# Kernel tuning notes

Measured on AMD Instinct MI355X. Metric: run time of the kernel, lower is better.

Reference implementation:

```python
import jax, jax.numpy as jnp
import numpy as np

B, S, D, DS = 8, 2048, 1024, 128
TEMP = 1.0
C = 8.0


def setup_inputs() -> dict:
    key = jax.random.key(0)
    ks = jax.random.split(key, 8)
    s_in = 1.0 / np.sqrt(D)
    s_st = 1.0 / np.sqrt(DS)
    return {
        "x": jax.random.normal(ks[0], (B, S, D), jnp.float32),
        "W_k": jax.random.normal(ks[1], (DS, D), jnp.float32) * s_in,
        "W_v": jax.random.normal(ks[2], (DS, D), jnp.float32) * s_in,
        "W_q": jax.random.normal(ks[3], (DS, D), jnp.float32) * s_in,
        "W_alpha_w": jax.random.normal(ks[4], (DS, D), jnp.float32) * s_in,
        "W_alpha_b": jnp.zeros((DS,), jnp.float32),
        "lambda_param": jax.random.uniform(ks[5], (DS,), jnp.float32, 4.0, 9.0),
        "W_o": jax.random.normal(ks[6], (D, DS), jnp.float32) * s_st,
        "norm_weight": jnp.ones((DS,), jnp.float32),
    }


def _l2norm(z):
    # matches F.normalize(..., dim=-1) with eps=1e-12
    n = jnp.linalg.norm(z, axis=-1, keepdims=True)
    return z / jnp.maximum(n, 1e-12)


def reference(x, W_k, W_v, W_q, W_alpha_w, W_alpha_b, lambda_param, W_o, norm_weight):
    # projections
    k = _l2norm(x @ W_k.T)                      # [B,S,DS]
    v = x @ W_v.T                               # [B,S,DS]
    q = _l2norm(x @ W_q.T)                      # [B,S,DS]
    r = jax.nn.sigmoid(x @ W_alpha_w.T + W_alpha_b)
    log_a = jnp.log(jax.nn.sigmoid(lambda_param) + 1e-8)  # [DS]
    alpha = jnp.exp(C * r * log_a)              # [B,S,DS], data-dependent decay

    H0 = jnp.zeros((B, DS, DS), x.dtype)        # state indexed [b, k, v]

    def step(H, inp):
        k_t, v_t, q_t, a_t = inp                # each [B,DS]
        # surprise: prediction error against current state
        pred = jnp.einsum('bk,bkv->bv', q_t, H)
        err = jnp.sum((v_t - pred) ** 2, axis=-1, keepdims=True)  # [B,1]
        sur = jax.nn.sigmoid(err / (TEMP + 1e-6))                 # [B,1]
        # delta rule: k (x) v - k (x) (k^T H) = k (x) (v - k^T H)
        k_proj = jnp.einsum('bk,bkv->bv', k_t, H)
        delta = k_t[:, :, None] * (v_t - k_proj)[:, None, :]      # [B,DS,DS]
        a_e = a_t[:, :, None]                                     # decay on k-axis
        H = a_e * H + (1.0 - a_e) * (sur[:, :, None] * delta)
        y = jnp.einsum('bk,bkv->bv', q_t, H)
        return H, y

    seq = (k.transpose(1, 0, 2), v.transpose(1, 0, 2),
           q.transpose(1, 0, 2), alpha.transpose(1, 0, 2))
    _, ys = jax.lax.scan(step, H0, seq)         # ys: [S,B,DS]
    y = ys.transpose(1, 0, 2)                   # [B,S,DS]

    # RMSNorm (computed in fp32, like the torch module)
    yf = y.astype(jnp.float32)
    yn = yf * jax.lax.rsqrt(jnp.mean(yf * yf, axis=-1, keepdims=True) + 1e-6)
    yn = (yn * norm_weight).astype(y.dtype)
    return yn @ W_o.T                           # [B,S,D]
```

## Files before the change

### kernel.cpp

```cpp
#include <hip/hip_runtime.h>
#include <math.h>

#define S_LEN 2048
#define B_SZ 8
#define D_IN 1024
#define DS_ 128
#define INV_TEMP (1.0f/1.000001f)

__global__ __launch_bounds__(256) void proj_gemm(
    const float* __restrict__ X,
    const float* __restrict__ Wk, const float* __restrict__ Wv,
    const float* __restrict__ Wq, const float* __restrict__ Wa,
    float* __restrict__ P)
{
    __shared__ __align__(16) float As[32][68];
    __shared__ __align__(16) float Bs[32][68];
    const int tid = threadIdx.x;
    const int m0 = blockIdx.x * 64;
    const int n0 = blockIdx.y * 64;
    const int lr = tid >> 3;
    const int lk4 = tid & 7;

    const float* wrows[2];
#pragma unroll
    for (int i = 0; i < 2; i++) {
        int nn = n0 + lr + i * 32;
        const float* w;
        if      (nn < 128) w = Wk + (size_t)nn * D_IN;
        else if (nn < 256) w = Wv + (size_t)(nn - 128) * D_IN;
        else if (nn < 384) w = Wq + (size_t)(nn - 256) * D_IN;
        else               w = Wa + (size_t)(nn - 384) * D_IN;
        wrows[i] = w;
    }
    const int ty = tid >> 4, tx = tid & 15;
    float acc[4][4];
#pragma unroll
    for (int i = 0; i < 4; i++)
#pragma unroll
        for (int j = 0; j < 4; j++) acc[i][j] = 0.f;

    for (int k0 = 0; k0 < D_IN; k0 += 32) {
#pragma unroll
        for (int i = 0; i < 2; i++) {
            int m = lr + i * 32;
            float4 a4 = *(const float4*)(X + (size_t)(m0 + m) * D_IN + k0 + lk4 * 4);
            As[lk4*4+0][m] = a4.x; As[lk4*4+1][m] = a4.y;
            As[lk4*4+2][m] = a4.z; As[lk4*4+3][m] = a4.w;
            float4 b4 = *(const float4*)(wrows[i] + k0 + lk4 * 4);
            Bs[lk4*4+0][m] = b4.x; Bs[lk4*4+1][m] = b4.y;
            Bs[lk4*4+2][m] = b4.z; Bs[lk4*4+3][m] = b4.w;
        }
        __syncthreads();
#pragma unroll
        for (int kk = 0; kk < 32; kk++) {
            float4 a4 = *(const float4*)(&As[kk][ty * 4]);
            float4 b4 = *(const float4*)(&Bs[kk][tx * 4]);
            float a[4] = {a4.x, a4.y, a4.z, a4.w};
            float b[4] = {b4.x, b4.y, b4.z, b4.w};
#pragma unroll
            for (int i = 0; i < 4; i++)
#pragma unroll
                for (int j = 0; j < 4; j++)
                    acc[i][j] = fmaf(a[i], b[j], acc[i][j]);
        }
        __syncthreads();
    }
#pragma unroll
    for (int i = 0; i < 4; i++) {
        float4 o; o.x = acc[i][0]; o.y = acc[i][1]; o.z = acc[i][2]; o.w = acc[i][3];
        *(float4*)(P + (size_t)(m0 + ty * 4 + i) * 512 + n0 + tx * 4) = o;
    }
}

__global__ __launch_bounds__(128) void postproc(
    float* __restrict__ P, float* __restrict__ G,
    const float* __restrict__ bA, const float* __restrict__ lam)
{
    const int tok = blockIdx.x, i = threadIdx.x;
    float* row = P + (size_t)tok * 512;
    float kr = row[i], qr = row[256 + i], rr = row[384 + i];
    float ks = kr * kr, qs = qr * qr;
#pragma unroll
    for (int m = 1; m < 64; m <<= 1) { ks += __shfl_xor(ks, m); qs += __shfl_xor(qs, m); }
    __shared__ float sb[6];
    if ((i & 63) == 0) { sb[(i >> 6) * 2] = ks; sb[(i >> 6) * 2 + 1] = qs; }
    __syncthreads();
    float kinv = 1.0f / fmaxf(sqrtf(sb[0] + sb[2]), 1e-12f);
    float qinv = 1.0f / fmaxf(sqrtf(sb[1] + sb[3]), 1e-12f);
    float kn = kr * kinv, qn = qr * qinv;
    float sr = 1.0f / (1.0f + __expf(-(rr + bA[i])));
    float sl = 1.0f / (1.0f + __expf(-lam[i]));
    float la = logf(sl + 1e-8f);
    float al = __expf(8.0f * sr * la);
    row[i]       = kn;
    row[256 + i] = qn;
    row[384 + i] = al;
    float gi = qn * (1.0f - al) * kn;
#pragma unroll
    for (int m = 1; m < 64; m <<= 1) gi += __shfl_xor(gi, m);
    if ((i & 63) == 0) sb[4 + (i >> 6)] = gi;
    __syncthreads();
    if (i == 0) G[tok] = sb[4] + sb[5];
}

__global__ __launch_bounds__(512, 2) void recurrence(
    const float* __restrict__ P, const float* __restrict__ G, float* __restrict__ Y)
{
    const int b = blockIdx.x;
    const int tid = threadIdx.x;
    const int c = tid & 7;
    const int vp = tid >> 3;
    const int lane = tid & 63;
    const int wave = tid >> 6;

    __shared__ __align__(16) float Pbuf[3][808];
    __shared__ __align__(16) float errw[2][8];

    const float* Pb = P + (size_t)b * S_LEN * 512;
    const float* Gb = G + (size_t)b * S_LEN;
    float* Yb = Y + (size_t)b * S_LEN * DS_;

    float H0[16], H1[16];
#pragma unroll
    for (int j = 0; j < 16; j++) { H0[j] = 0.f; H1[j] = 0.f; }

    const bool isP = tid < 256;
    const bool isG = (tid == 256);
    int spos = 0;
    if (isP) {
        int i0 = tid * 2, sec = i0 >> 7, idx = i0 & 127;
        spos = sec * 160 + (idx >> 4) * 20 + (idx & 15);
    }
    const int voff = 160 + (vp >> 3) * 20 + ((2 * vp) & 15);

    float2 rp0, rp1; float rg0 = 0.f, rg1 = 0.f;
    if (isP) {
        rp0 = *(const float2*)(Pb + tid * 2);
        rp1 = *(const float2*)(Pb + 512 + tid * 2);
    }
    if (isG) { rg0 = Gb[0]; rg1 = Gb[1]; }
    if (isP) *(float2*)(&Pbuf[0][spos]) = rp0;
    if (isG) Pbuf[0][800] = rg0;
    __syncthreads();

#define DOTC(j, u, comp) { \
    float q_ = q4[j].comp, k_ = k4[j].comp, a_ = a4[j].comp; \
    float h0 = H0[(j)*4+(u)], h1 = H1[(j)*4+(u)]; \
    pr0 = fmaf(q_, h0, pr0); pr1 = fmaf(q_, h1, pr1); \
    kp0 = fmaf(k_, h0, kp0); kp1 = fmaf(k_, h1, kp1); \
    float qa_ = q_ * a_; \
    ya0 = fmaf(qa_, h0, ya0); ya1 = fmaf(qa_, h1, ya1); }

#define UPDC(j, u, comp) { \
    float k_ = k4[j].comp, a_ = a4[j].comp; \
    float t0 = k_ * sd0, t1 = k_ * sd1; \
    H0[(j)*4+(u)] = fmaf(a_, H0[(j)*4+(u)] - t0, t0); \
    H1[(j)*4+(u)] = fmaf(a_, H1[(j)*4+(u)] - t1, t1); }

#define STEP(T, PAR, RPS, RGS, RPL, RGL) { \
    float* cb = &Pbuf[(T) % 3][0]; \
    const float* bk = cb + c * 20; \
    float4 k4[4], q4[4], a4[4]; \
    _Pragma("unroll") for (int j = 0; j < 4; j++) { \
        k4[j] = *(const float4*)(bk + j * 4); \
        q4[j] = *(const float4*)(bk + 320 + j * 4); \
        a4[j] = *(const float4*)(bk + 480 + j * 4); } \
    float2 vt = *(const float2*)(cb + voff); \
    float g = cb[800]; \
    float pr0 = 0, pr1 = 0, kp0 = 0, kp1 = 0, ya0 = 0, ya1 = 0; \
    _Pragma("unroll") for (int j = 0; j < 4; j++) { \
        DOTC(j, 0, x) DOTC(j, 1, y) DOTC(j, 2, z) DOTC(j, 3, w) } \
    _Pragma("unroll") for (int m = 1; m <= 4; m <<= 1) { \
        pr0 += __shfl_xor(pr0, m); pr1 += __shfl_xor(pr1, m); \
        kp0 += __shfl_xor(kp0, m); kp1 += __shfl_xor(kp1, m); \
        ya0 += __shfl_xor(ya0, m); ya1 += __shfl_xor(ya1, m); } \
    float e0 = vt.x - pr0, e1 = vt.y - pr1; \
    float d0 = vt.x - kp0, d1 = vt.y - kp1; \
    float ep = fmaf(e0, e0, e1 * e1); \
    ep += __shfl_xor(ep, 8); ep += __shfl_xor(ep, 16); ep += __shfl_xor(ep, 32); \
    if (lane == 0) errw[PAR][wave] = ep; \
    if ((T) + 1 < S_LEN) { \
        if (isP) *(float2*)(&Pbuf[((T) + 1) % 3][spos]) = RPS; \
        if (isG) Pbuf[((T) + 1) % 3][800] = RGS; } \
    if ((T) + 2 < S_LEN) { \
        if (isP) RPL = *(const float2*)(Pb + (size_t)((T) + 2) * 512 + tid * 2); \
        if (isG) RGL = Gb[(T) + 2]; } \
    __syncthreads(); \
    float4 ea = *(const float4*)(&errw[PAR][0]); \
    float4 eb = *(const float4*)(&errw[PAR][4]); \
    float err = ((ea.x + ea.y) + (ea.z + ea.w)) + ((eb.x + eb.y) + (eb.z + eb.w)); \
    float sur = 1.0f / (1.0f + __expf(-err * INV_TEMP)); \
    float sd0 = sur * d0, sd1 = sur * d1; \
    if (c == 0) { \
        float2 yv; float sg = sur * g; \
        yv.x = fmaf(sg, d0, ya0); yv.y = fmaf(sg, d1, ya1); \
        *(float2*)(Yb + (size_t)(T) * DS_ + vp * 2) = yv; } \
    _Pragma("unroll") for (int j = 0; j < 4; j++) { \
        UPDC(j, 0, x) UPDC(j, 1, y) UPDC(j, 2, z) UPDC(j, 3, w) } \
}

    for (int t = 0; t < S_LEN; t += 2) {
        STEP(t,     0, rp1, rg1, rp0, rg0)
        STEP(t + 1, 1, rp0, rg0, rp1, rg1)
    }
#undef DOTC
#undef UPDC
#undef STEP
}

__global__ __launch_bounds__(128) void rmsnorm(
    const float* __restrict__ Y, const float* __restrict__ nw, float* __restrict__ Yn)
{
    const int tok = blockIdx.x, i = threadIdx.x;
    float y = Y[(size_t)tok * DS_ + i];
    float s = y * y;
#pragma unroll
    for (int m = 1; m < 64; m <<= 1) s += __shfl_xor(s, m);
    __shared__ float sb[2];
    if ((i & 63) == 0) sb[i >> 6] = s;
    __syncthreads();
    float ms = (sb[0] + sb[1]) * (1.0f / 128.0f);
    Yn[(size_t)tok * DS_ + i] = y * rsqrtf(ms + 1e-6f) * nw[i];
}

__global__ __launch_bounds__(256) void out_gemm(
    const float* __restrict__ Yn, const float* __restrict__ Wo, float* __restrict__ Out)
{
    __shared__ __align__(16) float As[32][68];
    __shared__ __align__(16) float Bs[32][68];
    const int tid = threadIdx.x;
    const int m0 = blockIdx.x * 64;
    const int n0 = blockIdx.y * 64;
    const int lr = tid >> 3;
    const int lk4 = tid & 7;
    const int ty = tid >> 4, tx = tid & 15;
    float acc[4][4];
#pragma unroll
    for (int i = 0; i < 4; i++)
#pragma unroll
        for (int j = 0; j < 4; j++) acc[i][j] = 0.f;

    for (int k0 = 0; k0 < DS_; k0 += 32) {
#pragma unroll
        for (int i = 0; i < 2; i++) {
            int m = lr + i * 32;
            float4 a4 = *(const float4*)(Yn + (size_t)(m0 + m) * DS_ + k0 + lk4 * 4);
            As[lk4*4+0][m] = a4.x; As[lk4*4+1][m] = a4.y;
            As[lk4*4+2][m] = a4.z; As[lk4*4+3][m] = a4.w;
            float4 b4 = *(const float4*)(Wo + (size_t)(n0 + m) * DS_ + k0 + lk4 * 4);
            Bs[lk4*4+0][m] = b4.x; Bs[lk4*4+1][m] = b4.y;
            Bs[lk4*4+2][m] = b4.z; Bs[lk4*4+3][m] = b4.w;
        }
        __syncthreads();
#pragma unroll
        for (int kk = 0; kk < 32; kk++) {
            float4 a4 = *(const float4*)(&As[kk][ty * 4]);
            float4 b4 = *(const float4*)(&Bs[kk][tx * 4]);
            float a[4] = {a4.x, a4.y, a4.z, a4.w};
            float b[4] = {b4.x, b4.y, b4.z, b4.w};
#pragma unroll
            for (int i = 0; i < 4; i++)
#pragma unroll
                for (int j = 0; j < 4; j++)
                    acc[i][j] = fmaf(a[i], b[j], acc[i][j]);
        }
        __syncthreads();
    }
#pragma unroll
    for (int i = 0; i < 4; i++) {
        float4 o; o.x = acc[i][0]; o.y = acc[i][1]; o.z = acc[i][2]; o.w = acc[i][3];
        *(float4*)(Out + (size_t)(m0 + ty * 4 + i) * 1024 + n0 + tx * 4) = o;
    }
}

extern "C" void kernel_launch(void* const* d_in, const int* in_sizes, int n_in,
                              void* d_out, int out_size, void* d_ws, size_t ws_size,
                              hipStream_t stream)
{
    const float* x   = (const float*)d_in[0];
    const float* Wk  = (const float*)d_in[1];
    const float* Wv  = (const float*)d_in[2];
    const float* Wq  = (const float*)d_in[3];
    const float* Waw = (const float*)d_in[4];
    const float* Wab = (const float*)d_in[5];
    const float* lam = (const float*)d_in[6];
    const float* Wo  = (const float*)d_in[7];
    const float* nw  = (const float*)d_in[8];
    float* out = (float*)d_out;

    const size_t NTOK = (size_t)B_SZ * S_LEN;
    float* P  = (float*)d_ws;
    float* Y  = P + NTOK * 512;
    float* Yn = Y + NTOK * DS_;
    float* G  = Yn + NTOK * DS_;

    proj_gemm<<<dim3(NTOK / 64, 512 / 64), 256, 0, stream>>>(x, Wk, Wv, Wq, Waw, P);
    postproc<<<NTOK, 128, 0, stream>>>(P, G, Wab, lam);
    recurrence<<<B_SZ, 512, 0, stream>>>(P, G, Y);
    rmsnorm<<<NTOK, 128, 0, stream>>>(Y, nw, Yn);
    out_gemm<<<dim3(NTOK / 64, 1024 / 64), 256, 0, stream>>>(Yn, Wo, out);
}
```

Before: 3.003 ms.

## Precompute q*alpha and k*(1-alpha) and remap recurrence thread layout to 16x4

postproc now also writes per-token q*alpha, k*(1-alpha) and the gate scalar into a second buffer, so the recurrence no longer forms these products each step. The recurrence changes its thread mapping from 8 k-chunks by 2 v columns to 16 k-chunks by 4 v columns, with the H slice held as float4 registers, a padded shared-memory layout, and the decay/weight loads moved after the error reduction. rmsnorm writes in place to drop a buffer. The cost is more global traffic per step and longer shuffle reductions (16 lanes instead of 8).

```diff
diff --git a/kernel.cpp b/kernel.cpp
--- a/kernel.cpp
+++ b/kernel.cpp
@@ -6,6 +6,8 @@
 #define D_IN 1024
 #define DS_ 128
 #define INV_TEMP (1.0f/1.000001f)
+#define QROW 260
+#define LBUF 1092
 
 __global__ __launch_bounds__(256) void proj_gemm(
     const float* __restrict__ X,
@@ -73,7 +75,7 @@
 }
 
 __global__ __launch_bounds__(128) void postproc(
-    float* __restrict__ P, float* __restrict__ G,
+    float* __restrict__ P, float* __restrict__ Q2,
     const float* __restrict__ bA, const float* __restrict__ lam)
 {
     const int tok = blockIdx.x, i = threadIdx.x;
@@ -92,124 +94,130 @@
     float sl = 1.0f / (1.0f + __expf(-lam[i]));
     float la = logf(sl + 1e-8f);
     float al = __expf(8.0f * sr * la);
-    row[i]       = kn;
-    row[256 + i] = qn;
-    row[384 + i] = al;
+    row[i] = kn; row[256 + i] = qn; row[384 + i] = al;
+    float* q2 = Q2 + (size_t)tok * QROW;
+    q2[i] = qn * al;
+    q2[128 + i] = kn * (1.0f - al);
     float gi = qn * (1.0f - al) * kn;
 #pragma unroll
     for (int m = 1; m < 64; m <<= 1) gi += __shfl_xor(gi, m);
     if ((i & 63) == 0) sb[4 + (i >> 6)] = gi;
     __syncthreads();
-    if (i == 0) G[tok] = sb[4] + sb[5];
+    if (i == 0) q2[256] = sb[4] + sb[5];
 }
 
 __global__ __launch_bounds__(512, 2) void recurrence(
-    const float* __restrict__ P, const float* __restrict__ G, float* __restrict__ Y)
+    const float* __restrict__ P, const float* __restrict__ Q2, float* __restrict__ Y)
 {
     const int b = blockIdx.x;
     const int tid = threadIdx.x;
-    const int c = tid & 7;
-    const int vp = tid >> 3;
+    const int c = tid & 15;
+    const int vp = tid >> 4;
     const int lane = tid & 63;
     const int wave = tid >> 6;
-
-    __shared__ __align__(16) float Pbuf[3][808];
+    const int co = c * 12;
+
+    __shared__ __align__(16) float Pbuf[3][LBUF];
     __shared__ __align__(16) float errw[2][8];
 
     const float* Pb = P + (size_t)b * S_LEN * 512;
-    const float* Gb = G + (size_t)b * S_LEN;
+    const float* Qb = Q2 + (size_t)b * S_LEN * QROW;
     float* Yb = Y + (size_t)b * S_LEN * DS_;
 
-    float H0[16], H1[16];
-#pragma unroll
-    for (int j = 0; j < 16; j++) { H0[j] = 0.f; H1[j] = 0.f; }
-
-    const bool isP = tid < 256;
-    const bool isG = (tid == 256);
-    int spos = 0;
-    if (isP) {
-        int i0 = tid * 2, sec = i0 >> 7, idx = i0 & 127;
-        spos = sec * 160 + (idx >> 4) * 20 + (idx & 15);
-    }
-    const int voff = 160 + (vp >> 3) * 20 + ((2 * vp) & 15);
-
-    float2 rp0, rp1; float rg0 = 0.f, rg1 = 0.f;
-    if (isP) {
-        rp0 = *(const float2*)(Pb + tid * 2);
-        rp1 = *(const float2*)(Pb + 512 + tid * 2);
-    }
-    if (isG) { rg0 = Gb[0]; rg1 = Gb[1]; }
-    if (isP) *(float2*)(&Pbuf[0][spos]) = rp0;
-    if (isG) Pbuf[0][800] = rg0;
+    float4 H0={0,0,0,0},H1={0,0,0,0},H2={0,0,0,0},H3={0,0,0,0},
+           H4={0,0,0,0},H5={0,0,0,0},H6={0,0,0,0},H7={0,0,0,0};
+
+    const bool isS = tid < 385;
+    int spos = 0; const float* src = nullptr; int sstr = 0;
+    if (tid < 256) {
+        int i = tid * 2, s = i >> 7, idx = i & 127, cp = (idx >> 3) * 12 + (idx & 7);
+        spos = (s == 0) ? cp : (s == 1) ? (960 + idx) : (s == 2) ? (192 + cp) : (576 + cp);
+        src = Pb + i; sstr = 512;
+    } else if (tid < 385) {
+        int i2 = (tid - 256) * 2, s = i2 >> 7, idx = i2 & 127, cp = (idx >> 3) * 12 + (idx & 7);
+        spos = (tid == 384) ? 1088 : ((s == 0) ? (384 + cp) : (768 + cp));
+        src = Qb + i2; sstr = QROW;
+    }
+
+    float2 r0 = {0.f, 0.f}, r1 = {0.f, 0.f};
+    if (isS) { r0 = *(const float2*)(src); r1 = *(const float2*)(src + sstr); }
+    if (isS) *(float2*)(&Pbuf[0][spos]) = r0;
     __syncthreads();
 
-#define DOTC(j, u, comp) { \
-    float q_ = q4[j].comp, k_ = k4[j].comp, a_ = a4[j].comp; \
-    float h0 = H0[(j)*4+(u)], h1 = H1[(j)*4+(u)]; \
-    pr0 = fmaf(q_, h0, pr0); pr1 = fmaf(q_, h1, pr1); \
-    kp0 = fmaf(k_, h0, kp0); kp1 = fmaf(k_, h1, kp1); \
-    float qa_ = q_ * a_; \
-    ya0 = fmaf(qa_, h0, ya0); ya1 = fmaf(qa_, h1, ya1); }
-
-#define UPDC(j, u, comp) { \
-    float k_ = k4[j].comp, a_ = a4[j].comp; \
-    float t0 = k_ * sd0, t1 = k_ * sd1; \
-    H0[(j)*4+(u)] = fmaf(a_, H0[(j)*4+(u)] - t0, t0); \
-    H1[(j)*4+(u)] = fmaf(a_, H1[(j)*4+(u)] - t1, t1); }
-
-#define STEP(T, PAR, RPS, RGS, RPL, RGL) { \
+#define RED16(v4) { _Pragma("unroll") for (int m_ = 1; m_ < 16; m_ <<= 1) { \
+    v4.x += __shfl_xor(v4.x, m_); v4.y += __shfl_xor(v4.y, m_); \
+    v4.z += __shfl_xor(v4.z, m_); v4.w += __shfl_xor(v4.w, m_); } }
+
+#define DOTJ(qs, ks, zs, Hj) { \
+    pr.x = fmaf(qs, Hj.x, pr.x); pr.y = fmaf(qs, Hj.y, pr.y); \
+    pr.z = fmaf(qs, Hj.z, pr.z); pr.w = fmaf(qs, Hj.w, pr.w); \
+    kp.x = fmaf(ks, Hj.x, kp.x); kp.y = fmaf(ks, Hj.y, kp.y); \
+    kp.z = fmaf(ks, Hj.z, kp.z); kp.w = fmaf(ks, Hj.w, kp.w); \
+    ya.x = fmaf(zs, Hj.x, ya.x); ya.y = fmaf(zs, Hj.y, ya.y); \
+    ya.z = fmaf(zs, Hj.z, ya.z); ya.w = fmaf(zs, Hj.w, ya.w); }
+
+#define UPDJ(as_, ws_, Hj) { \
+    Hj.x = fmaf(as_, Hj.x, ws_ * sd.x); Hj.y = fmaf(as_, Hj.y, ws_ * sd.y); \
+    Hj.z = fmaf(as_, Hj.z, ws_ * sd.z); Hj.w = fmaf(as_, Hj.w, ws_ * sd.w); }
+
+#define STEP(T, PAR, RS_, RL_) { \
     float* cb = &Pbuf[(T) % 3][0]; \
-    const float* bk = cb + c * 20; \
-    float4 k4[4], q4[4], a4[4]; \
-    _Pragma("unroll") for (int j = 0; j < 4; j++) { \
-        k4[j] = *(const float4*)(bk + j * 4); \
-        q4[j] = *(const float4*)(bk + 320 + j * 4); \
-        a4[j] = *(const float4*)(bk + 480 + j * 4); } \
-    float2 vt = *(const float2*)(cb + voff); \
-    float g = cb[800]; \
-    float pr0 = 0, pr1 = 0, kp0 = 0, kp1 = 0, ya0 = 0, ya1 = 0; \
-    _Pragma("unroll") for (int j = 0; j < 4; j++) { \
-        DOTC(j, 0, x) DOTC(j, 1, y) DOTC(j, 2, z) DOTC(j, 3, w) } \
-    _Pragma("unroll") for (int m = 1; m <= 4; m <<= 1) { \
-        pr0 += __shfl_xor(pr0, m); pr1 += __shfl_xor(pr1, m); \
-        kp0 += __shfl_xor(kp0, m); kp1 += __shfl_xor(kp1, m); \
-        ya0 += __shfl_xor(ya0, m); ya1 += __shfl_xor(ya1, m); } \
-    float e0 = vt.x - pr0, e1 = vt.y - pr1; \
-    float d0 = vt.x - kp0, d1 = vt.y - kp1; \
-    float ep = fmaf(e0, e0, e1 * e1); \
-    ep += __shfl_xor(ep, 8); ep += __shfl_xor(ep, 16); ep += __shfl_xor(ep, 32); \
+    const float4 k0 = *(const float4*)(cb + co); \
+    const float4 k1 = *(const float4*)(cb + co + 4); \
+    const float4 q0 = *(const float4*)(cb + 192 + co); \
+    const float4 q1 = *(const float4*)(cb + 192 + co + 4); \
+    const float4 z0 = *(const float4*)(cb + 384 + co); \
+    const float4 z1 = *(const float4*)(cb + 384 + co + 4); \
+    const float4 vt = *(const float4*)(cb + 960 + vp * 4); \
+    const float g = cb[1088]; \
+    float4 pr = {0,0,0,0}, kp = {0,0,0,0}, ya = {0,0,0,0}; \
+    DOTJ(q0.x, k0.x, z0.x, H0) DOTJ(q0.y, k0.y, z0.y, H1) \
+    DOTJ(q0.z, k0.z, z0.z, H2) DOTJ(q0.w, k0.w, z0.w, H3) \
+    DOTJ(q1.x, k1.x, z1.x, H4) DOTJ(q1.y, k1.y, z1.y, H5) \
+    DOTJ(q1.z, k1.z, z1.z, H6) DOTJ(q1.w, k1.w, z1.w, H7) \
+    RED16(pr) RED16(kp) RED16(ya) \
+    float4 d4; d4.x = vt.x - kp.x; d4.y = vt.y - kp.y; \
+    d4.z = vt.z - kp.z; d4.w = vt.w - kp.w; \
+    float ex = vt.x - pr.x, ey = vt.y - pr.y, ez = vt.z - pr.z, ew = vt.w - pr.w; \
+    float ep = fmaf(ex, ex, fmaf(ey, ey, fmaf(ez, ez, ew * ew))); \
+    ep += __shfl_xor(ep, 16); ep += __shfl_xor(ep, 32); \
     if (lane == 0) errw[PAR][wave] = ep; \
-    if ((T) + 1 < S_LEN) { \
-        if (isP) *(float2*)(&Pbuf[((T) + 1) % 3][spos]) = RPS; \
-        if (isG) Pbuf[((T) + 1) % 3][800] = RGS; } \
-    if ((T) + 2 < S_LEN) { \
-        if (isP) RPL = *(const float2*)(Pb + (size_t)((T) + 2) * 512 + tid * 2); \
-        if (isG) RGL = Gb[(T) + 2]; } \
+    if ((T) + 1 < S_LEN && isS) *(float2*)(&Pbuf[((T) + 1) % 3][spos]) = RS_; \
+    if ((T) + 2 < S_LEN && isS) RL_ = *(const float2*)(src + (size_t)((T) + 2) * sstr); \
+    const float4 a0 = *(const float4*)(cb + 576 + co); \
+    const float4 a1 = *(const float4*)(cb + 576 + co + 4); \
+    const float4 w0 = *(const float4*)(cb + 768 + co); \
+    const float4 w1 = *(const float4*)(cb + 768 + co + 4); \
     __syncthreads(); \
-    float4 ea = *(const float4*)(&errw[PAR][0]); \
-    float4 eb = *(const float4*)(&errw[PAR][4]); \
+    const float4 ea = *(const float4*)(&errw[PAR][0]); \
+    const float4 eb = *(const float4*)(&errw[PAR][4]); \
     float err = ((ea.x + ea.y) + (ea.z + ea.w)) + ((eb.x + eb.y) + (eb.z + eb.w)); \
     float sur = 1.0f / (1.0f + __expf(-err * INV_TEMP)); \
-    float sd0 = sur * d0, sd1 = sur * d1; \
+    float4 sd; sd.x = sur * d4.x; sd.y = sur * d4.y; \
+    sd.z = sur * d4.z; sd.w = sur * d4.w; \
     if (c == 0) { \
-        float2 yv; float sg = sur * g; \
-        yv.x = fmaf(sg, d0, ya0); yv.y = fmaf(sg, d1, ya1); \
-        *(float2*)(Yb + (size_t)(T) * DS_ + vp * 2) = yv; } \
-    _Pragma("unroll") for (int j = 0; j < 4; j++) { \
-        UPDC(j, 0, x) UPDC(j, 1, y) UPDC(j, 2, z) UPDC(j, 3, w) } \
+        float sg = sur * g; float4 y4; \
+        y4.x = fmaf(sg, d4.x, ya.x); y4.y = fmaf(sg, d4.y, ya.y); \
+        y4.z = fmaf(sg, d4.z, ya.z); y4.w = fmaf(sg, d4.w, ya.w); \
+        *(float4*)(Yb + (size_t)(T) * DS_ + vp * 4) = y4; } \
+    UPDJ(a0.x, w0.x, H0) UPDJ(a0.y, w0.y, H1) \
+    UPDJ(a0.z, w0.z, H2) UPDJ(a0.w, w0.w, H3) \
+    UPDJ(a1.x, w1.x, H4) UPDJ(a1.y, w1.y, H5) \
+    UPDJ(a1.z, w1.z, H6) UPDJ(a1.w, w1.w, H7) \
 }
 
     for (int t = 0; t < S_LEN; t += 2) {
-        STEP(t,     0, rp1, rg1, rp0, rg0)
-        STEP(t + 1, 1, rp0, rg0, rp1, rg1)
-    }
-#undef DOTC
-#undef UPDC
+        STEP(t,     0, r1, r0)
+        STEP(t + 1, 1, r0, r1)
+    }
+#undef RED16
+#undef DOTJ
+#undef UPDJ
 #undef STEP
 }
 
 __global__ __launch_bounds__(128) void rmsnorm(
-    const float* __restrict__ Y, const float* __restrict__ nw, float* __restrict__ Yn)
+    float* __restrict__ Y, const float* __restrict__ nw)
 {
     const int tok = blockIdx.x, i = threadIdx.x;
     float y = Y[(size_t)tok * DS_ + i];
@@ -220,7 +228,7 @@
     if ((i & 63) == 0) sb[i >> 6] = s;
     __syncthreads();
     float ms = (sb[0] + sb[1]) * (1.0f / 128.0f);
-    Yn[(size_t)tok * DS_ + i] = y * rsqrtf(ms + 1e-6f) * nw[i];
+    Y[(size_t)tok * DS_ + i] = y * rsqrtf(ms + 1e-6f) * nw[i];
 }
 
 __global__ __launch_bounds__(256) void out_gemm(
@@ -290,13 +298,12 @@
 
     const size_t NTOK = (size_t)B_SZ * S_LEN;
     float* P  = (float*)d_ws;
-    float* Y  = P + NTOK * 512;
-    float* Yn = Y + NTOK * DS_;
-    float* G  = Yn + NTOK * DS_;
+    float* Q2 = P + NTOK * 512;
+    float* Y  = Q2 + NTOK * QROW;
 
     proj_gemm<<<dim3(NTOK / 64, 512 / 64), 256, 0, stream>>>(x, Wk, Wv, Wq, Waw, P);
-    postproc<<<NTOK, 128, 0, stream>>>(P, G, Wab, lam);
-    recurrence<<<B_SZ, 512, 0, stream>>>(P, G, Y);
-    rmsnorm<<<NTOK, 128, 0, stream>>>(Y, nw, Yn);
-    out_gemm<<<dim3(NTOK / 64, 1024 / 64), 256, 0, stream>>>(Yn, Wo, out);
-}
+    postproc<<<NTOK, 128, 0, stream>>>(P, Q2, Wab, lam);
+    recurrence<<<B_SZ, 512, 0, stream>>>(P, Q2, Y);
+    rmsnorm<<<NTOK, 128, 0, stream>>>(Y, nw);
+    out_gemm<<<dim3(NTOK / 64, 1024 / 64), 256, 0, stream>>>(Y, Wo, out);
+}
```

New measurement: 3.780 ms. 1.26x slower.
